# Kernel optimization log

Measured on AMD Instinct MI355X. Metric: run time of the kernel, lower is better.

The kernel has to match this reference:

```python
import jax, jax.numpy as jnp
import numpy as np

B, N, D, H = 4, 2048, 256, 8
DH = D // H  # 32
EPS = 1e-5


def layernorm(x, g, b):
    mu = jnp.mean(x, axis=-1, keepdims=True)
    var = jnp.mean(jnp.square(x - mu), axis=-1, keepdims=True)
    return (x - mu) * jax.lax.rsqrt(var + EPS) * g + b


def setup_inputs() -> dict:
    key = jax.random.key(0)
    ks = jax.random.split(key, 16)
    s = 1.0 / np.sqrt(D)
    p = lambda k: jax.random.uniform(k, (D, D), jnp.float32, -s, s)
    return {
        "qdt": jax.random.normal(ks[0], (B, N, D), jnp.float32),
        "boxes": jax.random.normal(ks[1], (B, N, D), jnp.float32),
        "mask": jax.random.randint(ks[2], (N, N), 0, 2, jnp.int32),
        "Wq": p(ks[3]), "bq": jnp.zeros((D,), jnp.float32),
        "Wk": p(ks[4]), "bk": jnp.zeros((D,), jnp.float32),
        "Wv": p(ks[5]), "bv": jnp.zeros((D,), jnp.float32),
        "Wo": p(ks[6]), "bo": jnp.zeros((D,), jnp.float32),
        "W1": p(ks[7]), "b1": jnp.zeros((D,), jnp.float32),
        "W2": p(ks[8]), "b2": jnp.zeros((D,), jnp.float32),
        "g1": jnp.ones((D,), jnp.float32), "be1": jnp.zeros((D,), jnp.float32),
        "g2": jnp.ones((D,), jnp.float32), "be2": jnp.zeros((D,), jnp.float32),
    }


def reference(qdt, boxes, mask, Wq, bq, Wk, bk, Wv, bv, Wo, bo,
              W1, b1, W2, b2, g1, be1, g2, be2):
    # q = k = tgt = boxes + qdt  (dropout in eval mode -> identity)
    x = boxes + qdt  # [B,N,D]
    q = (x @ Wq + bq).reshape(B, N, H, DH)
    k = (x @ Wk + bk).reshape(B, N, H, DH)
    v = (x @ Wv + bv).reshape(B, N, H, DH)
    scores = jnp.einsum('bqhd,bkhd->bhqk', q, k) / np.sqrt(DH)
    # masked_fill(mask==0, -inf) then sigmoid  ==  sigmoid gated to 0 where masked
    attn = jnp.where(mask.astype(bool)[None, None, :, :],
                     jax.nn.sigmoid(scores), 0.0)
    o = jnp.einsum('bhqk,bkhd->bqhd', attn, v).reshape(B, N, D)
    attn_out = o @ Wo + bo
    tgt = layernorm(x + attn_out, g1, be1)
    ff = jax.nn.relu(tgt @ W1 + b1) @ W2 + b2
    tgt = layernorm(tgt + ff, g2, be2)
    return tgt
```

## Files before the change

kernel.cpp:

```cpp
#include <hip/hip_runtime.h>
#include <hip/hip_bf16.h>

typedef unsigned short u16;
typedef unsigned int u32;
typedef __attribute__((ext_vector_type(8))) short bf16x8;
typedef __attribute__((ext_vector_type(4))) float f32x4;

#define BB 4
#define NN 2048
#define DD 256
#define HH 8
#define LAMBDA 0.17677669529f

__device__ inline u16 bfu(float f) {
  __hip_bfloat16 h = __float2bfloat16(f);
  return *reinterpret_cast<u16*>(&h);
}
__device__ inline bf16x8 asfrag(uint4 v) { return __builtin_bit_cast(bf16x8, v); }

__global__ __launch_bounds__(256) void prep_kernel(
    const float* __restrict__ qdt, const float* __restrict__ boxes,
    const int* __restrict__ mask,
    const float* __restrict__ Wq, const float* __restrict__ Wk, const float* __restrict__ Wv,
    const float* __restrict__ Wo, const float* __restrict__ W1, const float* __restrict__ W2,
    const float* __restrict__ bq, const float* __restrict__ bk, const float* __restrict__ bv,
    float* __restrict__ x, u16* __restrict__ xb, unsigned char* __restrict__ m8,
    u16* __restrict__ wqkvT, u16* __restrict__ woT, u16* __restrict__ w1T, u16* __restrict__ w2T,
    float* __restrict__ bqkv) {
  const int bid = blockIdx.x, t = threadIdx.x;
  if (bid < 2048) {
    int i = bid * 256 + t;
    float4 a = ((const float4*)qdt)[i];
    float4 b = ((const float4*)boxes)[i];
    float4 v = make_float4(a.x + b.x, a.y + b.y, a.z + b.z, a.w + b.w);
    ((float4*)x)[i] = v;
    ((ushort4*)xb)[i] = make_ushort4(bfu(v.x), bfu(v.y), bfu(v.z), bfu(v.w));
  } else if (bid < 6144) {
    int i = (bid - 2048) * 256 + t;
    int4 m = ((const int4*)mask)[i];
    ((uchar4*)m8)[i] = make_uchar4((unsigned char)m.x, (unsigned char)m.y,
                                   (unsigned char)m.z, (unsigned char)m.w);
  } else {
    int i = (bid - 6144) * 256 + t;
    if (i < 196608) {
      int n = i >> 8, k = i & 255;
      const float* src = (n < 256) ? Wq : (n < 512 ? Wk : Wv);
      wqkvT[i] = bfu(src[k * 256 + (n & 255)]);
    } else if (i < 262144) {
      int j = i - 196608; int n = j >> 8, k = j & 255;
      woT[j] = bfu(Wo[k * 256 + n]);
    } else if (i < 327680) {
      int j = i - 262144; int n = j >> 8, k = j & 255;
      w1T[j] = bfu(W1[k * 256 + n]);
    } else if (i < 393216) {
      int j = i - 327680; int n = j >> 8, k = j & 255;
      w2T[j] = bfu(W2[k * 256 + n]);
    } else if (i < 393984) {
      int n = i - 393216;
      bqkv[n] = (n < 256) ? bq[n] : (n < 512 ? bk[n - 256] : bv[n - 512]);
    }
  }
}

#define GEMM_BODY()                                                              \
  __shared__ u16 At[64][264];                                                    \
  __shared__ u16 Bs[64][264];                                                    \
  const int m0 = blockIdx.x * 64;                                                \
  const int n0 = blockIdx.y * 64;                                                \
  const int t = threadIdx.x;                                                     \
  {                                                                              \
    const int row = t >> 2, cb = (t & 3) * 64;                                   \
    const u16* ga = A  + (size_t)(m0 + row) * 256 + cb;                          \
    const u16* gb = Bt + (size_t)(n0 + row) * 256 + cb;                          \
    _Pragma("unroll")                                                            \
    for (int i = 0; i < 8; ++i) {                                                \
      *(int4*)&At[row][cb + i * 8] = *(const int4*)(ga + i * 8);                 \
      *(int4*)&Bs[row][cb + i * 8] = *(const int4*)(gb + i * 8);                 \
    }                                                                            \
  }                                                                              \
  __syncthreads();                                                               \
  const int w = t >> 6, l = t & 63, g = l >> 4, c = l & 15;                      \
  f32x4 acc[4] = {};                                                             \
  _Pragma("unroll")                                                              \
  for (int kk = 0; kk < 256; kk += 32) {                                         \
    bf16x8 af = *(const bf16x8*)&At[w * 16 + c][kk + g * 8];                     \
    _Pragma("unroll")                                                            \
    for (int j = 0; j < 4; ++j) {                                                \
      bf16x8 bfr = *(const bf16x8*)&Bs[j * 16 + c][kk + g * 8];                  \
      acc[j] = __builtin_amdgcn_mfma_f32_16x16x32_bf16(af, bfr, acc[j], 0, 0, 0);\
    }                                                                            \
  }

__global__ __launch_bounds__(256) void gemm_qk_kernel(
    const u16* __restrict__ A, const u16* __restrict__ Bt, const float* __restrict__ bias,
    u16* __restrict__ qout, u16* __restrict__ kout) {
  GEMM_BODY()
  if (n0 < 256) {
#pragma unroll
    for (int j = 0; j < 4; ++j)
#pragma unroll
      for (int r = 0; r < 4; ++r) {
        int m = m0 + w * 16 + g * 4 + r, n = n0 + j * 16 + c;
        qout[(size_t)m * 256 + n] = bfu((acc[j][r] + bias[n]) * LAMBDA);
      }
  } else {
#pragma unroll
    for (int j = 0; j < 4; ++j)
#pragma unroll
      for (int r = 0; r < 4; ++r) {
        int m = m0 + w * 16 + g * 4 + r, n = n0 + j * 16 + c;
        int ch = n - 256;
        kout[(size_t)((m >> 11) * 8 + (ch >> 5)) * 65536 + (size_t)(m & 2047) * 32 + (ch & 31)]
            = bfu(acc[j][r] + bias[n]);
      }
  }
}

__global__ __launch_bounds__(256) void gemm_vt_kernel(
    const u16* __restrict__ A, const u16* __restrict__ Bt, const float* __restrict__ bias,
    u16* __restrict__ vtout) {
  GEMM_BODY()
#pragma unroll
  for (int j = 0; j < 4; ++j)
#pragma unroll
    for (int r = 0; r < 4; ++r) {
      int m = m0 + w * 16 + g * 4 + r;
      int n = n0 + j * 16 + c;
      vtout[(size_t)m * 8192 + n] = bfu(acc[j][r] + bias[m]);
    }
}

template<int MODE>
__global__ __launch_bounds__(256) void gemm256_kernel(
    const u16* __restrict__ A, const u16* __restrict__ Bt,
    const float* __restrict__ bias, const float* res,
    void* out, int ldout) {
  GEMM_BODY()
#pragma unroll
  for (int j = 0; j < 4; ++j)
#pragma unroll
    for (int r = 0; r < 4; ++r) {
      int m = m0 + w * 16 + g * 4 + r;
      int n = n0 + j * 16 + c;
      float v = acc[j][r] + bias[n];
      size_t oi = (size_t)m * ldout + n;
      if (MODE == 1) {
        ((u16*)out)[oi] = bfu(v > 0.f ? v : 0.f);
      } else {
        ((float*)out)[oi] = v + res[(size_t)m * 256 + n];
      }
    }
}

__global__ __launch_bounds__(256) void attn_kernel(
    const u16* __restrict__ qb,
    const u16* __restrict__ kb,
    const u16* __restrict__ vtb,
    const unsigned char* __restrict__ m8,
    u16* __restrict__ ob) {
  __shared__ u32 Klds[2][64][20];
  __shared__ u32 Vlds[2][32][36];
  __shared__ unsigned char Mlds[2][64][64];
  __shared__ u32 Plds[4][16][36];

  const int bid = blockIdx.x;
  const int qt = bid & 31, h = (bid >> 5) & 7, b = bid >> 8;
  const int q0 = qt * 64;
  const int t = threadIdx.x, w = t >> 6, l = t & 63, g = l >> 4, c = l & 15;

  const bf16x8 qf = asfrag(*(const uint4*)(qb + (size_t)(b * NN + q0 + 16 * w + c) * 256 + h * 32 + 8 * g));
  f32x4 oacc[2] = {};

  const int srowK = t >> 2, ssegK = t & 3;
  const int srowV = t >> 3, ssegV = t & 7;
  const u16* kg = kb + (size_t)(b * 8 + h) * 65536 + srowK * 32 + ssegK * 8;
  const u16* vg = vtb + (size_t)(h * 32 + srowV) * 8192 + (size_t)b * NN + ssegV * 8;
  const unsigned char* mg = m8 + (size_t)(q0 + srowK) * NN + ssegK * 16;

  const int mb0 = (16 * ssegK + 8 * (srowK & 7)) & 63;
  const int mb1 = (mb0 + 8) & 63;

  uint4 krg = *(const uint4*)kg;
  uint4 vrg = *(const uint4*)vg;
  uint4 mrg = *(const uint4*)mg;
  *(uint4*)&Klds[0][srowK][ssegK * 4] = krg;
  *(uint4*)&Vlds[0][srowV][ssegV * 4] = vrg;
  *(uint2*)&Mlds[0][srowK][mb0] = make_uint2(mrg.x, mrg.y);
  *(uint2*)&Mlds[0][srowK][mb1] = make_uint2(mrg.z, mrg.w);
  __syncthreads();

  const f32x4 zf = {0.f, 0.f, 0.f, 0.f};
  u32* Pw = &Plds[w][0][0];

  for (int it = 0; it < 32; ++it) {
    const int cur = it & 1;
    if (it < 31) {
      const int kt = (it + 1) * 64;
      krg = *(const uint4*)(kg + (size_t)kt * 32);
      vrg = *(const uint4*)(vg + kt);
      mrg = *(const uint4*)(mg + kt);
    }
#pragma unroll
    for (int tt = 0; tt < 4; ++tt) {
      bf16x8 kf = asfrag(*(const uint4*)&Klds[cur][16 * tt + c][4 * g]);
      f32x4 s = __builtin_amdgcn_mfma_f32_16x16x32_bf16(kf, qf, zf, 0, 0, 0);
      u32 mdw = *(const u32*)&Mlds[cur][16 * w + c][(16 * tt + 4 * g + 8 * (c & 7)) & 63];
      float mf0 = (float)(mdw & 0xffu);
      float mf1 = (float)((mdw >> 8) & 0xffu);
      float mf2 = (float)((mdw >> 16) & 0xffu);
      float mf3 = (float)(mdw >> 24);
      float p0 = mf0 * __builtin_amdgcn_rcpf(1.f + __expf(-s[0]));
      float p1 = mf1 * __builtin_amdgcn_rcpf(1.f + __expf(-s[1]));
      float p2 = mf2 * __builtin_amdgcn_rcpf(1.f + __expf(-s[2]));
      float p3 = mf3 * __builtin_amdgcn_rcpf(1.f + __expf(-s[3]));
      u32 w0, w1;
      asm("v_cvt_pk_bf16_f32 %0, %1, %2" : "=v"(w0) : "v"(p0), "v"(p1));
      asm("v_cvt_pk_bf16_f32 %0, %1, %2" : "=v"(w1) : "v"(p2), "v"(p3));
      *(uint2*)&Pw[c * 36 + 8 * tt + 2 * g] = make_uint2(w0, w1);
    }
    asm volatile("s_waitcnt lgkmcnt(0)" ::: "memory");
    __builtin_amdgcn_sched_barrier(0);
#pragma unroll
    for (int kk = 0; kk < 2; ++kk) {
      bf16x8 pf = asfrag(*(const uint4*)&Pw[c * 36 + 16 * kk + 4 * g]);
#pragma unroll
      for (int d0 = 0; d0 < 2; ++d0) {
        bf16x8 vf = asfrag(*(const uint4*)&Vlds[cur][16 * d0 + c][16 * kk + 4 * g]);
        oacc[d0] = __builtin_amdgcn_mfma_f32_16x16x32_bf16(pf, vf, oacc[d0], 0, 0, 0);
      }
    }
    if (it < 31) {
      *(uint4*)&Klds[cur ^ 1][srowK][ssegK * 4] = krg;
      *(uint4*)&Vlds[cur ^ 1][srowV][ssegV * 4] = vrg;
      *(uint2*)&Mlds[cur ^ 1][srowK][mb0] = make_uint2(mrg.x, mrg.y);
      *(uint2*)&Mlds[cur ^ 1][srowK][mb1] = make_uint2(mrg.z, mrg.w);
    }
    __syncthreads();
  }

  const size_t obase = (size_t)(b * NN + q0 + 16 * w) * 256 + h * 32;
#pragma unroll
  for (int d0 = 0; d0 < 2; ++d0)
#pragma unroll
    for (int r = 0; r < 4; ++r)
      ob[obase + (size_t)(4 * g + r) * 256 + 16 * d0 + c] = bfu(oacc[d0][r]);
}

template<int WB>
__global__ __launch_bounds__(256) void ln_kernel(const float* y,
    const float* __restrict__ gam, const float* __restrict__ bet,
    float* outf, u16* outb) {
  const int row = blockIdx.x * 4 + (threadIdx.x >> 6);
  const int l = threadIdx.x & 63;
  const float4 v = ((const float4*)(y + (size_t)row * DD))[l];
  float s1 = v.x + v.y + v.z + v.w;
  float s2 = v.x * v.x + v.y * v.y + v.z * v.z + v.w * v.w;
#pragma unroll
  for (int off = 1; off < 64; off <<= 1) {
    s1 += __shfl_xor(s1, off);
    s2 += __shfl_xor(s2, off);
  }
  const float mean = s1 * (1.f / DD);
  const float var = s2 * (1.f / DD) - mean * mean;
  const float inv = rsqrtf(var + 1e-5f);
  const float4 gg = ((const float4*)gam)[l];
  const float4 bb = ((const float4*)bet)[l];
  float o0 = (v.x - mean) * inv * gg.x + bb.x;
  float o1 = (v.y - mean) * inv * gg.y + bb.y;
  float o2 = (v.z - mean) * inv * gg.z + bb.z;
  float o3 = (v.w - mean) * inv * gg.w + bb.w;
  ((float4*)(outf + (size_t)row * DD))[l] = make_float4(o0, o1, o2, o3);
  if (WB) {
    ((ushort4*)(outb + (size_t)row * DD))[l] = make_ushort4(bfu(o0), bfu(o1), bfu(o2), bfu(o3));
  }
}

extern "C" void kernel_launch(void* const* d_in, const int* in_sizes, int n_in,
                              void* d_out, int out_size, void* d_ws, size_t ws_size,
                              hipStream_t stream) {
  const float* qdt   = (const float*)d_in[0];
  const float* boxes = (const float*)d_in[1];
  const int*   mask  = (const int*)d_in[2];
  const float* Wq = (const float*)d_in[3];
  const float* bq = (const float*)d_in[4];
  const float* Wk = (const float*)d_in[5];
  const float* bk = (const float*)d_in[6];
  const float* Wv = (const float*)d_in[7];
  const float* bv = (const float*)d_in[8];
  const float* Wo = (const float*)d_in[9];
  const float* bo = (const float*)d_in[10];
  const float* W1 = (const float*)d_in[11];
  const float* b1 = (const float*)d_in[12];
  const float* W2 = (const float*)d_in[13];
  const float* b2 = (const float*)d_in[14];
  const float* g1  = (const float*)d_in[15];
  const float* be1 = (const float*)d_in[16];
  const float* g2  = (const float*)d_in[17];
  const float* be2 = (const float*)d_in[18];

  char* ws = (char*)d_ws;
  float* x     = (float*)(ws + 0);
  u16*   xb    = (u16*)  (ws + 8388608);
  u16*   qbuf  = (u16*)  (ws + 12582912);
  u16*   kbuf  = (u16*)  (ws + 16777216);
  u16*   vtbuf = (u16*)  (ws + 20971520);
  u16*   obuf  = (u16*)  (ws + 25165824);
  float* y1    = (float*)(ws + 29360128);
  u16*   t1b   = (u16*)  (ws + 37748736);
  u16*   f1b   = (u16*)  (ws + 41943040);
  u16*   wqkvT = (u16*)  (ws + 46137344);
  u16*   woT   = (u16*)  (ws + 46530560);
  u16*   w1T   = (u16*)  (ws + 46661632);
  u16*   w2T   = (u16*)  (ws + 46792704);
  float* bqkv  = (float*)(ws + 46923776);
  unsigned char* m8 = (unsigned char*)(ws + 46926848);

  prep_kernel<<<7683, 256, 0, stream>>>(qdt, boxes, mask, Wq, Wk, Wv, Wo, W1, W2,
                                        bq, bk, bv, x, xb, m8,
                                        wqkvT, woT, w1T, w2T, bqkv);
  gemm_qk_kernel<<<dim3(128, 8), 256, 0, stream>>>(xb, wqkvT, bqkv, qbuf, kbuf);
  gemm_vt_kernel<<<dim3(4, 128), 256, 0, stream>>>(wqkvT + 512 * 256, xb, bqkv + 512, vtbuf);
  attn_kernel<<<1024, 256, 0, stream>>>(qbuf, kbuf, vtbuf, m8, obuf);
  gemm256_kernel<2><<<dim3(128, 4), 256, 0, stream>>>(obuf, woT, bo, x, y1, 256);
  ln_kernel<1><<<2048, 256, 0, stream>>>(y1, g1, be1, y1, t1b);
  gemm256_kernel<1><<<dim3(128, 4), 256, 0, stream>>>(t1b, w1T, b1, nullptr, f1b, 256);
  gemm256_kernel<2><<<dim3(128, 4), 256, 0, stream>>>(f1b, w2T, b2, y1, x, 256);
  ln_kernel<0><<<2048, 256, 0, stream>>>(x, g2, be2, (float*)d_out, nullptr);
}
```

Measured before the change: 127.3 us.

## Fuse output projection, layernorms and FFN into a single tail kernel

Replaces the five tail launches (Wo GEMM, LN1, W1 GEMM, W2 GEMM, LN2) with one kernel in which each wave keeps a 16-row tile in registers and LDS across all three GEMMs and both layernorms. The residual x is stored in a permuted per-row layout so each lane can read its MFMA output columns as contiguous float4s. This removes the intermediate global round trips for y1, t1b and f1b and the launch gaps between them. The cost is only 128 blocks of 256 threads with launch_bounds(256,1), which leaves many CUs idle and uses low occupancy, and every wave streams the full weight matrices from global memory.

```diff
diff --git a/kernel.cpp b/kernel.cpp
--- a/kernel.cpp
+++ b/kernel.cpp
@@ -24,17 +24,22 @@
     const float* __restrict__ Wq, const float* __restrict__ Wk, const float* __restrict__ Wv,
     const float* __restrict__ Wo, const float* __restrict__ W1, const float* __restrict__ W2,
     const float* __restrict__ bq, const float* __restrict__ bk, const float* __restrict__ bv,
-    float* __restrict__ x, u16* __restrict__ xb, unsigned char* __restrict__ m8,
+    float* __restrict__ xp, u16* __restrict__ xb, unsigned char* __restrict__ m8,
     u16* __restrict__ wqkvT, u16* __restrict__ woT, u16* __restrict__ w1T, u16* __restrict__ w2T,
     float* __restrict__ bqkv) {
   const int bid = blockIdx.x, t = threadIdx.x;
   if (bid < 2048) {
     int i = bid * 256 + t;
+    int row = i >> 6, q = i & 63;
     float4 a = ((const float4*)qdt)[i];
     float4 b = ((const float4*)boxes)[i];
     float4 v = make_float4(a.x + b.x, a.y + b.y, a.z + b.z, a.w + b.w);
-    ((float4*)x)[i] = v;
     ((ushort4*)xb)[i] = make_ushort4(bfu(v.x), bfu(v.y), bfu(v.z), bfu(v.w));
+    float* xr = xp + (size_t)row * 256;
+    xr[((4*q+0) & 15) * 16 + ((4*q+0) >> 4)] = v.x;
+    xr[((4*q+1) & 15) * 16 + ((4*q+1) >> 4)] = v.y;
+    xr[((4*q+2) & 15) * 16 + ((4*q+2) >> 4)] = v.z;
+    xr[((4*q+3) & 15) * 16 + ((4*q+3) >> 4)] = v.w;
   } else if (bid < 6144) {
     int i = (bid - 2048) * 256 + t;
     int4 m = ((const int4*)mask)[i];
@@ -130,28 +135,6 @@
     }
 }
 
-template<int MODE>
-__global__ __launch_bounds__(256) void gemm256_kernel(
-    const u16* __restrict__ A, const u16* __restrict__ Bt,
-    const float* __restrict__ bias, const float* res,
-    void* out, int ldout) {
-  GEMM_BODY()
-#pragma unroll
-  for (int j = 0; j < 4; ++j)
-#pragma unroll
-    for (int r = 0; r < 4; ++r) {
-      int m = m0 + w * 16 + g * 4 + r;
-      int n = n0 + j * 16 + c;
-      float v = acc[j][r] + bias[n];
-      size_t oi = (size_t)m * ldout + n;
-      if (MODE == 1) {
-        ((u16*)out)[oi] = bfu(v > 0.f ? v : 0.f);
-      } else {
-        ((float*)out)[oi] = v + res[(size_t)m * 256 + n];
-      }
-    }
-}
-
 __global__ __launch_bounds__(256) void attn_kernel(
     const u16* __restrict__ qb,
     const u16* __restrict__ kb,
@@ -246,32 +229,162 @@
       ob[obase + (size_t)(4 * g + r) * 256 + 16 * d0 + c] = bfu(oacc[d0][r]);
 }
 
-template<int WB>
-__global__ __launch_bounds__(256) void ln_kernel(const float* y,
-    const float* __restrict__ gam, const float* __restrict__ bet,
-    float* outf, u16* outb) {
-  const int row = blockIdx.x * 4 + (threadIdx.x >> 6);
-  const int l = threadIdx.x & 63;
-  const float4 v = ((const float4*)(y + (size_t)row * DD))[l];
-  float s1 = v.x + v.y + v.z + v.w;
-  float s2 = v.x * v.x + v.y * v.y + v.z * v.z + v.w * v.w;
-#pragma unroll
-  for (int off = 1; off < 64; off <<= 1) {
-    s1 += __shfl_xor(s1, off);
-    s2 += __shfl_xor(s2, off);
-  }
-  const float mean = s1 * (1.f / DD);
-  const float var = s2 * (1.f / DD) - mean * mean;
-  const float inv = rsqrtf(var + 1e-5f);
-  const float4 gg = ((const float4*)gam)[l];
-  const float4 bb = ((const float4*)bet)[l];
-  float o0 = (v.x - mean) * inv * gg.x + bb.x;
-  float o1 = (v.y - mean) * inv * gg.y + bb.y;
-  float o2 = (v.z - mean) * inv * gg.z + bb.z;
-  float o3 = (v.w - mean) * inv * gg.w + bb.w;
-  ((float4*)(outf + (size_t)row * DD))[l] = make_float4(o0, o1, o2, o3);
-  if (WB) {
-    ((ushort4*)(outb + (size_t)row * DD))[l] = make_ushort4(bfu(o0), bfu(o1), bfu(o2), bfu(o3));
+__global__ __launch_bounds__(256, 1) void tail_kernel(
+    const u16* __restrict__ obuf, const u16* __restrict__ woT,
+    const u16* __restrict__ w1T, const u16* __restrict__ w2T,
+    const float* __restrict__ xp,
+    const float* __restrict__ bo, const float* __restrict__ b1, const float* __restrict__ b2,
+    const float* __restrict__ g1, const float* __restrict__ be1,
+    const float* __restrict__ g2, const float* __restrict__ be2,
+    float* __restrict__ out) {
+  __shared__ u16 At[4][16][264];
+  const int t = threadIdx.x, w = t >> 6, l = t & 63, g = l >> 4, c = l & 15;
+  const int m0 = blockIdx.x * 64 + w * 16;
+  u16 (*A)[264] = At[w];
+  const f32x4 zf4 = {0.f, 0.f, 0.f, 0.f};
+
+  {
+    const int rr = l >> 5, ss = l & 31;
+#pragma unroll
+    for (int i = 0; i < 8; ++i) {
+      uint4 v = *(const uint4*)(obuf + (size_t)(m0 + 2 * i + rr) * 256 + ss * 8);
+      *(uint4*)&A[2 * i + rr][ss * 8] = v;
+    }
+  }
+  asm volatile("s_waitcnt lgkmcnt(0)" ::: "memory");
+  __builtin_amdgcn_sched_barrier(0);
+
+  f32x4 acc[16], t1[16];
+
+#pragma unroll
+  for (int j = 0; j < 16; ++j) acc[j] = zf4;
+#pragma unroll
+  for (int kk = 0; kk < 256; kk += 32) {
+    bf16x8 af = *(const bf16x8*)&A[c][kk + 8 * g];
+#pragma unroll
+    for (int j = 0; j < 16; ++j) {
+      bf16x8 bfr = asfrag(*(const uint4*)(woT + (size_t)(16 * j + c) * 256 + kk + 8 * g));
+      acc[j] = __builtin_amdgcn_mfma_f32_16x16x32_bf16(af, bfr, acc[j], 0, 0, 0);
+    }
+  }
+  float bov[16];
+#pragma unroll
+  for (int j = 0; j < 16; ++j) bov[j] = bo[16 * j + c];
+  float s1[4], s2[4];
+#pragma unroll
+  for (int r = 0; r < 4; ++r) {
+    const float* xrow = xp + (size_t)(m0 + 4 * g + r) * 256 + c * 16;
+    float4 xq0 = ((const float4*)xrow)[0], xq1 = ((const float4*)xrow)[1];
+    float4 xq2 = ((const float4*)xrow)[2], xq3 = ((const float4*)xrow)[3];
+    float xa[16] = {xq0.x, xq0.y, xq0.z, xq0.w, xq1.x, xq1.y, xq1.z, xq1.w,
+                    xq2.x, xq2.y, xq2.z, xq2.w, xq3.x, xq3.y, xq3.z, xq3.w};
+    float a1 = 0.f, a2 = 0.f;
+#pragma unroll
+    for (int j = 0; j < 16; ++j) {
+      float z = acc[j][r] + bov[j] + xa[j];
+      t1[j][r] = z;
+      a1 += z; a2 += z * z;
+    }
+    s1[r] = a1; s2[r] = a2;
+  }
+#pragma unroll
+  for (int r = 0; r < 4; ++r) {
+#pragma unroll
+    for (int off = 1; off < 16; off <<= 1) {
+      s1[r] += __shfl_xor(s1[r], off);
+      s2[r] += __shfl_xor(s2[r], off);
+    }
+  }
+  float mean[4], inv[4];
+#pragma unroll
+  for (int r = 0; r < 4; ++r) {
+    mean[r] = s1[r] * (1.f / 256.f);
+    inv[r] = rsqrtf(s2[r] * (1.f / 256.f) - mean[r] * mean[r] + 1e-5f);
+  }
+  asm volatile("" ::: "memory");
+  __builtin_amdgcn_sched_barrier(0);
+#pragma unroll
+  for (int j = 0; j < 16; ++j) {
+    const int n = 16 * j + c;
+    const float gv = g1[n], bev = be1[n];
+#pragma unroll
+    for (int r = 0; r < 4; ++r) {
+      float v = (t1[j][r] - mean[r]) * inv[r] * gv + bev;
+      t1[j][r] = v;
+      A[4 * g + r][n] = bfu(v);
+    }
+  }
+  asm volatile("s_waitcnt lgkmcnt(0)" ::: "memory");
+  __builtin_amdgcn_sched_barrier(0);
+
+#pragma unroll
+  for (int j = 0; j < 16; ++j) acc[j] = zf4;
+#pragma unroll
+  for (int kk = 0; kk < 256; kk += 32) {
+    bf16x8 af = *(const bf16x8*)&A[c][kk + 8 * g];
+#pragma unroll
+    for (int j = 0; j < 16; ++j) {
+      bf16x8 bfr = asfrag(*(const uint4*)(w1T + (size_t)(16 * j + c) * 256 + kk + 8 * g));
+      acc[j] = __builtin_amdgcn_mfma_f32_16x16x32_bf16(af, bfr, acc[j], 0, 0, 0);
+    }
+  }
+  asm volatile("" ::: "memory");
+  __builtin_amdgcn_sched_barrier(0);
+#pragma unroll
+  for (int j = 0; j < 16; ++j) {
+    const int n = 16 * j + c;
+    const float bv = b1[n];
+#pragma unroll
+    for (int r = 0; r < 4; ++r) {
+      float v = acc[j][r] + bv;
+      A[4 * g + r][n] = bfu(v > 0.f ? v : 0.f);
+    }
+  }
+  asm volatile("s_waitcnt lgkmcnt(0)" ::: "memory");
+  __builtin_amdgcn_sched_barrier(0);
+
+#pragma unroll
+  for (int j = 0; j < 16; ++j) acc[j] = zf4;
+#pragma unroll
+  for (int kk = 0; kk < 256; kk += 32) {
+    bf16x8 af = *(const bf16x8*)&A[c][kk + 8 * g];
+#pragma unroll
+    for (int j = 0; j < 16; ++j) {
+      bf16x8 bfr = asfrag(*(const uint4*)(w2T + (size_t)(16 * j + c) * 256 + kk + 8 * g));
+      acc[j] = __builtin_amdgcn_mfma_f32_16x16x32_bf16(af, bfr, acc[j], 0, 0, 0);
+    }
+  }
+  float b2v[16];
+#pragma unroll
+  for (int j = 0; j < 16; ++j) b2v[j] = b2[16 * j + c];
+#pragma unroll
+  for (int r = 0; r < 4; ++r) {
+    float a1 = 0.f, a2 = 0.f;
+#pragma unroll
+    for (int j = 0; j < 16; ++j) {
+      float z = acc[j][r] + b2v[j] + t1[j][r];
+      t1[j][r] = z;
+      a1 += z; a2 += z * z;
+    }
+    s1[r] = a1; s2[r] = a2;
+  }
+#pragma unroll
+  for (int r = 0; r < 4; ++r) {
+#pragma unroll
+    for (int off = 1; off < 16; off <<= 1) {
+      s1[r] += __shfl_xor(s1[r], off);
+      s2[r] += __shfl_xor(s2[r], off);
+    }
+    mean[r] = s1[r] * (1.f / 256.f);
+    inv[r] = rsqrtf(s2[r] * (1.f / 256.f) - mean[r] * mean[r] + 1e-5f);
+  }
+#pragma unroll
+  for (int j = 0; j < 16; ++j) {
+    const int n = 16 * j + c;
+    const float gv = g2[n], bev = be2[n];
+#pragma unroll
+    for (int r = 0; r < 4; ++r)
+      out[(size_t)(m0 + 4 * g + r) * 256 + n] = (t1[j][r] - mean[r]) * inv[r] * gv + bev;
   }
 }
 
@@ -299,15 +412,12 @@
   const float* be2 = (const float*)d_in[18];
 
   char* ws = (char*)d_ws;
-  float* x     = (float*)(ws + 0);
+  float* xp    = (float*)(ws + 0);
   u16*   xb    = (u16*)  (ws + 8388608);
   u16*   qbuf  = (u16*)  (ws + 12582912);
   u16*   kbuf  = (u16*)  (ws + 16777216);
   u16*   vtbuf = (u16*)  (ws + 20971520);
   u16*   obuf  = (u16*)  (ws + 25165824);
-  float* y1    = (float*)(ws + 29360128);
-  u16*   t1b   = (u16*)  (ws + 37748736);
-  u16*   f1b   = (u16*)  (ws + 41943040);
   u16*   wqkvT = (u16*)  (ws + 46137344);
   u16*   woT   = (u16*)  (ws + 46530560);
   u16*   w1T   = (u16*)  (ws + 46661632);
@@ -316,14 +426,11 @@
   unsigned char* m8 = (unsigned char*)(ws + 46926848);
 
   prep_kernel<<<7683, 256, 0, stream>>>(qdt, boxes, mask, Wq, Wk, Wv, Wo, W1, W2,
-                                        bq, bk, bv, x, xb, m8,
+                                        bq, bk, bv, xp, xb, m8,
                                         wqkvT, woT, w1T, w2T, bqkv);
   gemm_qk_kernel<<<dim3(128, 8), 256, 0, stream>>>(xb, wqkvT, bqkv, qbuf, kbuf);
   gemm_vt_kernel<<<dim3(4, 128), 256, 0, stream>>>(wqkvT + 512 * 256, xb, bqkv + 512, vtbuf);
   attn_kernel<<<1024, 256, 0, stream>>>(qbuf, kbuf, vtbuf, m8, obuf);
-  gemm256_kernel<2><<<dim3(128, 4), 256, 0, stream>>>(obuf, woT, bo, x, y1, 256);
-  ln_kernel<1><<<2048, 256, 0, stream>>>(y1, g1, be1, y1, t1b);
-  gemm256_kernel<1><<<dim3(128, 4), 256, 0, stream>>>(t1b, w1T, b1, nullptr, f1b, 256);
-  gemm256_kernel<2><<<dim3(128, 4), 256, 0, stream>>>(f1b, w2T, b2, y1, x, 256);
-  ln_kernel<0><<<2048, 256, 0, stream>>>(x, g2, be2, (float*)d_out, nullptr);
-}
+  tail_kernel<<<128, 256, 0, stream>>>(obuf, woT, w1T, w2T, xp,
+                                       bo, b1, b2, g1, be1, g2, be2, (float*)d_out);
+}
```

Result: slower. 190.2 us (+49.4%).
